# Kernel optimization log

Hardware: AMD Instinct MI355X
Metric: run time of the kernel (lower is better)

## Reference

```python
import jax, jax.numpy as jnp
import numpy as np

B, C, D, H, W = 8, 1, 160, 160, 160
SPATIAL_AXES = (2, 3, 4)  # axial, coronal, sagittal map to dims D, H, W


def setup_inputs() -> dict:
    key = jax.random.key(0)
    k1, _ = jax.random.split(key)
    x = jax.random.normal(k1, (B, C, D, H, W), dtype=jnp.float32)
    log_sigma = jnp.zeros((3,), dtype=jnp.float32)  # log(initial_sigma=1.0)
    return {"x": x, "log_sigma": log_sigma}


def reference(x, log_sigma):
    # For each spatial axis: adjacent-slice diff, squared distance summed over
    # channel + remaining spatial dims (per batch, per slice-pair), RBF kernel,
    # then -mean over (batch, slice-pairs). Equivalent to the original
    # sum_i(-mean_b(k_i)) / (n_slices - 1) since mean is linear.
    sigma = jnp.exp(log_sigma)
    total = jnp.float32(0.0)
    for i, ax in enumerate(SPATIAL_AXES):
        d = jnp.diff(x, axis=ax)  # [B, C, ...] with S-1 along ax
        reduce_dims = tuple(a for a in range(5) if a not in (0, ax))
        sq = jnp.sum(d * d, axis=reduce_dims)  # [B, S-1]
        k = jnp.exp(-sq / (2.0 * sigma[i] ** 2))
        total = total + (-jnp.mean(k))
    return total / jnp.float32(len(SPATIAL_AXES))
```

## Files before the change

kernel.cpp:

```cpp
#include <hip/hip_runtime.h>


constexpr int Wd4 = 40;
constexpr int SLICE4 = 6400;
constexpr long BSTR4 = 160L * 6400;
constexpr int NB = 8;
constexpr int NPAIR = 159;
constexpr int NKEY = 3 * NB * NPAIR;
constexpr int SLOT = 200;
constexpr int NBLK = NB * 160;
constexpr int PART_OFF = NBLK * SLOT;
constexpr int NFIN = 60;

__device__ __forceinline__ float sq4(const float4& a, const float4& c) {
    float e0 = a.x - c.x, e1 = a.y - c.y, e2 = a.z - c.z, e3 = a.w - c.w;
    return e0 * e0 + e1 * e1 + e2 * e2 + e3 * e3;
}

__global__ __launch_bounds__(320) void diff3_kernel(const float* __restrict__ x,
                                                    float* __restrict__ ws) {
    __shared__ float lds[1504];

    const int t = threadIdx.x;
    const int bid = blockIdx.x;
    const int b = bid / 160;
    const int r2 = bid % 160;
    const int ds = r2 / 5;
    const int hc = r2 % 5;
    const int d0 = ds * 5, h0 = hc * 32;
    const bool lastSeg = (ds == 31);

    const int c4 = t % 40;
    const int rp = t / 40;
    const int lane = t & 63;
    const int wv = t >> 6;
    const bool hOK = !(hc == 4 && rp == 7);
    const bool sOK = (c4 < 39);
    const bool fixB = (lane == 63) && sOK;

    const float4* base = (const float4*)x + (size_t)b * BSTR4 + (size_t)d0 * SLICE4
                       + (size_t)(h0 + 4 * rp) * Wd4 + c4;

    float aW[4] = {0.f, 0.f, 0.f, 0.f};
    float aH[4] = {0.f, 0.f, 0.f, 0.f};
    float aD[5] = {0.f, 0.f, 0.f, 0.f, 0.f};
    float4 p0, p1, p2, p3;

#pragma unroll
    for (int it = 0; it < 5; ++it) {
        const float4* sp = base + it * SLICE4;
        const float4 v0 = sp[0];
        const float4 v1 = sp[Wd4];
        const float4 v2 = sp[2 * Wd4];
        const float4 v3 = sp[3 * Wd4];
        float4 hv;
        if (hOK) hv = sp[4 * Wd4];
        float bx0 = 0.f, bx1 = 0.f, bx2 = 0.f, bx3 = 0.f;
        if (fixB) {
            bx0 = ((const float*)(sp))[4];
            bx1 = ((const float*)(sp + Wd4))[4];
            bx2 = ((const float*)(sp + 2 * Wd4))[4];
            bx3 = ((const float*)(sp + 3 * Wd4))[4];
        }
        float s0 = __shfl_down(v0.x, 1, 64); if (fixB) s0 = bx0;
        float s1 = __shfl_down(v1.x, 1, 64); if (fixB) s1 = bx1;
        float s2 = __shfl_down(v2.x, 1, 64); if (fixB) s2 = bx2;
        float s3 = __shfl_down(v3.x, 1, 64); if (fixB) s3 = bx3;

        float dw;
        dw = v0.y - v0.x; aW[0] += dw * dw;
        dw = v0.z - v0.y; aW[1] += dw * dw;
        dw = v0.w - v0.z; aW[2] += dw * dw;
        dw = v1.y - v1.x; aW[0] += dw * dw;
        dw = v1.z - v1.y; aW[1] += dw * dw;
        dw = v1.w - v1.z; aW[2] += dw * dw;
        dw = v2.y - v2.x; aW[0] += dw * dw;
        dw = v2.z - v2.y; aW[1] += dw * dw;
        dw = v2.w - v2.z; aW[2] += dw * dw;
        dw = v3.y - v3.x; aW[0] += dw * dw;
        dw = v3.z - v3.y; aW[1] += dw * dw;
        dw = v3.w - v3.z; aW[2] += dw * dw;
        if (sOK) {
            dw = s0 - v0.w; aW[3] += dw * dw;
            dw = s1 - v1.w; aW[3] += dw * dw;
            dw = s2 - v2.w; aW[3] += dw * dw;
            dw = s3 - v3.w; aW[3] += dw * dw;
        }
        aH[0] += sq4(v1, v0);
        aH[1] += sq4(v2, v1);
        aH[2] += sq4(v3, v2);
        if (hOK) aH[3] += sq4(hv, v3);
        if (it > 0)
            aD[it - 1] += sq4(v0, p0) + sq4(v1, p1) + sq4(v2, p2) + sq4(v3, p3);
        p0 = v0; p1 = v1; p2 = v2; p3 = v3;
    }
    if (!lastSeg) {
        const float4* sp = base + 5 * SLICE4;
        aD[4] = sq4(sp[0], p0) + sq4(sp[Wd4], p1) + sq4(sp[2 * Wd4], p2) + sq4(sp[3 * Wd4], p3);
    }

#pragma unroll
    for (int j = 0; j < 4; ++j) lds[(4 * rp + j) * 41 + c4] = aH[j];
#pragma unroll
    for (int j = 0; j < 5; ++j) {
        float dd = aD[j];
        for (int off = 32; off > 0; off >>= 1) dd += __shfl_down(dd, off, 64);
        if (lane == 0) lds[1472 + j * 5 + wv] = dd;
    }
    __syncthreads();
    float hsum = 0.f, dsum = 0.f;
    if (t < 32) {
        const float* src = &lds[t * 41];
        for (int i = 0; i < 40; ++i) hsum += src[i];
    }
    if (t < 5) {
        for (int w2 = 0; w2 < 5; ++w2) dsum += lds[1472 + t * 5 + w2];
    }
    __syncthreads();
#pragma unroll
    for (int j = 0; j < 4; ++j) lds[(4 * c4 + j) * 9 + rp] = aW[j];
    __syncthreads();
    float wsum = 0.f;
    if (t < 160) {
        const float* src = &lds[t * 9];
        for (int i = 0; i < 8; ++i) wsum += src[i];
    }
    float* slot = ws + (size_t)bid * SLOT;
    if (t < 5)   slot[t] = dsum;
    if (t < 32)  slot[5 + t] = hsum;
    if (t < 160) slot[37 + t] = wsum;
}

__global__ __launch_bounds__(64) void reduce_kernel(const float* __restrict__ ws,
                                                    const float* __restrict__ log_sigma,
                                                    float* __restrict__ part) {
    const int gk = blockIdx.x * 64 + threadIdx.x;
    float kv = 0.f;
    if (gk < NKEY) {
        const int a = gk / (NB * NPAIR);
        const int rem = gk % (NB * NPAIR);
        const int b = rem / NPAIR;
        const int k = rem % NPAIR;
        const float f = -0.5f * expf(-2.f * log_sigma[a]);
        const float* bb = ws + (size_t)b * 160 * SLOT;
        float val = 0.f;
        if (a == 0) {
            const int ds = k / 5, j = k % 5;
            const float* p = bb + (size_t)(ds * 5) * SLOT + j;
            for (int hc = 0; hc < 5; ++hc) val += p[hc * SLOT];
        } else if (a == 1) {
            const int hc = k / 32, kk = k % 32;
            const float* p = bb + (size_t)hc * SLOT + 5 + kk;
            for (int ds = 0; ds < 32; ++ds) val += p[(size_t)(ds * 5) * SLOT];
        } else {
            const float* p = bb + 37 + k;
            for (int i = 0; i < 160; ++i) val += p[(size_t)i * SLOT];
        }
        kv = expf(val * f);
    }
    for (int off = 32; off > 0; off >>= 1) kv += __shfl_down(kv, off, 64);
    if (threadIdx.x == 0) part[blockIdx.x] = kv;
}

__global__ __launch_bounds__(64) void final_kernel(const float* __restrict__ part,
                                                   float* __restrict__ out) {
    float v = (threadIdx.x < NFIN) ? part[threadIdx.x] : 0.f;
    for (int off = 32; off > 0; off >>= 1) v += __shfl_down(v, off, 64);
    if (threadIdx.x == 0) out[0] = -v / (float)NKEY;
}

extern "C" void kernel_launch(void* const* d_in, const int* in_sizes, int n_in,
                              void* d_out, int out_size, void* d_ws, size_t ws_size,
                              hipStream_t stream) {
    const float* x = (const float*)d_in[0];
    const float* log_sigma = (const float*)d_in[1];
    float* out = (float*)d_out;
    float* ws = (float*)d_ws;

    diff3_kernel<<<NBLK, 320, 0, stream>>>(x, ws);
    reduce_kernel<<<NFIN, 64, 0, stream>>>(ws, log_sigma, ws + PART_OFF);
    final_kernel<<<1, 64, 0, stream>>>(ws + PART_OFF, out);
}
```

Baseline: 196.5 us.

## Stage slices into LDS with async global_load_lds triple buffering and smaller tiles

Each block now works on a 16-row tile instead of a 32-row one, so there are twice as many blocks. Each D-slice is staged into a three-deep LDS ring with async global-to-LDS loads, using vmcnt waits and barriers so the next slices load while the current one is computed. The final reduction kernel is dropped: the reduce kernel atomically adds into the output, which the first kernel zeroes. This targets memory latency and one launch, at the cost of more LDS per block, more barriers, and a nondeterministic atomic sum order.

```diff
diff --git a/kernel.cpp b/kernel.cpp
--- a/kernel.cpp
+++ b/kernel.cpp
@@ -1,71 +1,93 @@
 #include <hip/hip_runtime.h>
 
 
-constexpr int Wd4 = 40;
-constexpr int SLICE4 = 6400;
-constexpr long BSTR4 = 160L * 6400;
+constexpr int WF = 160;
+constexpr int SLICEF = 160 * 160;
+constexpr long BSTRF = 160L * SLICEF;
 constexpr int NB = 8;
 constexpr int NPAIR = 159;
 constexpr int NKEY = 3 * NB * NPAIR;
-constexpr int SLOT = 200;
-constexpr int NBLK = NB * 160;
-constexpr int PART_OFF = NBLK * SLOT;
-constexpr int NFIN = 60;
+constexpr int SLOT = 184;
+constexpr int NTILE = NB * 32 * 10;
+constexpr int BUFF = 3840;
+constexpr int NRED = 60;
 
 __device__ __forceinline__ float sq4(const float4& a, const float4& c) {
     float e0 = a.x - c.x, e1 = a.y - c.y, e2 = a.z - c.z, e3 = a.w - c.w;
     return e0 * e0 + e1 * e1 + e2 * e2 + e3 * e3;
 }
 
-__global__ __launch_bounds__(320) void diff3_kernel(const float* __restrict__ x,
-                                                    float* __restrict__ ws) {
-    __shared__ float lds[1504];
+__device__ __forceinline__ void stage16(const float* g, float* l) {
+    __builtin_amdgcn_global_load_lds(
+        (const __attribute__((address_space(1))) void*)g,
+        (__attribute__((address_space(3))) void*)l, 16, 0, 0);
+}
+
+__device__ __forceinline__ void stage_slice(const float* gs, float* lb, int t, int hc) {
+    stage16(gs + t * 4, lb + t * 4);
+    stage16(gs + 1280 + t * 4, lb + 1280 + t * 4);
+    const int hoff = (hc == 9) ? 0 : 2560;
+    stage16(gs + hoff + (t % 40) * 4, lb + 2560 + t * 4);
+}
+
+__global__ __launch_bounds__(320, 4) void diff3_kernel(const float* __restrict__ x,
+                                                       float* __restrict__ ws,
+                                                       float* __restrict__ out) {
+    __shared__ float ldsf[3 * BUFF];
 
     const int t = threadIdx.x;
-    const int bid = blockIdx.x;
-    const int b = bid / 160;
-    const int r2 = bid % 160;
-    const int ds = r2 / 5;
-    const int hc = r2 % 5;
-    const int d0 = ds * 5, h0 = hc * 32;
+    const int tile = blockIdx.x;
+    const int b = tile / 320;
+    const int r2 = tile % 320;
+    const int ds = r2 / 10;
+    const int hc = r2 % 10;
+    const int d0 = ds * 5, h0 = hc * 16;
     const bool lastSeg = (ds == 31);
 
     const int c4 = t % 40;
     const int rp = t / 40;
     const int lane = t & 63;
     const int wv = t >> 6;
-    const bool hOK = !(hc == 4 && rp == 7);
     const bool sOK = (c4 < 39);
-    const bool fixB = (lane == 63) && sOK;
+    const bool hOK = !(hc == 9 && rp == 7);
 
-    const float4* base = (const float4*)x + (size_t)b * BSTR4 + (size_t)d0 * SLICE4
-                       + (size_t)(h0 + 4 * rp) * Wd4 + c4;
+    if (tile == 0 && t == 0) out[0] = 0.f;
+
+    const float* gs0 = x + (size_t)b * BSTRF + (size_t)d0 * SLICEF + (size_t)h0 * WF;
+
+    stage_slice(gs0, ldsf, t, hc);
+    stage_slice(gs0 + SLICEF, ldsf + BUFF, t, hc);
 
     float aW[4] = {0.f, 0.f, 0.f, 0.f};
-    float aH[4] = {0.f, 0.f, 0.f, 0.f};
+    float aH0 = 0.f, aH1 = 0.f;
     float aD[5] = {0.f, 0.f, 0.f, 0.f, 0.f};
-    float4 p0, p1, p2, p3;
+    float4 p0, p1;
+
+    const int r0 = 2 * rp, r1 = 2 * rp + 1;
 
 #pragma unroll
     for (int it = 0; it < 5; ++it) {
-        const float4* sp = base + it * SLICE4;
-        const float4 v0 = sp[0];
-        const float4 v1 = sp[Wd4];
-        const float4 v2 = sp[2 * Wd4];
-        const float4 v3 = sp[3 * Wd4];
+        if (it < 4 || !lastSeg) {
+            asm volatile("s_waitcnt vmcnt(3)" ::: "memory");
+        } else {
+            asm volatile("s_waitcnt vmcnt(0)" ::: "memory");
+        }
+        __builtin_amdgcn_s_barrier();
+        __builtin_amdgcn_sched_barrier(0);
+        if (it < 3 || (it == 3 && !lastSeg))
+            stage_slice(gs0 + (size_t)(it + 2) * SLICEF, ldsf + ((it + 2) % 3) * BUFF, t, hc);
+
+        const float* bp = ldsf + (it % 3) * BUFF;
+        const float4* b4 = (const float4*)bp;
+        const float4 v0 = b4[r0 * 40 + c4];
+        const float4 v1 = b4[r1 * 40 + c4];
         float4 hv;
-        if (hOK) hv = sp[4 * Wd4];
-        float bx0 = 0.f, bx1 = 0.f, bx2 = 0.f, bx3 = 0.f;
-        if (fixB) {
-            bx0 = ((const float*)(sp))[4];
-            bx1 = ((const float*)(sp + Wd4))[4];
-            bx2 = ((const float*)(sp + 2 * Wd4))[4];
-            bx3 = ((const float*)(sp + 3 * Wd4))[4];
+        if (hOK) hv = b4[(r0 + 2) * 40 + c4];
+        float s0 = 0.f, s1 = 0.f;
+        if (sOK) {
+            s0 = bp[r0 * WF + 4 * c4 + 4];
+            s1 = bp[r1 * WF + 4 * c4 + 4];
         }
-        float s0 = __shfl_down(v0.x, 1, 64); if (fixB) s0 = bx0;
-        float s1 = __shfl_down(v1.x, 1, 64); if (fixB) s1 = bx1;
-        float s2 = __shfl_down(v2.x, 1, 64); if (fixB) s2 = bx2;
-        float s3 = __shfl_down(v3.x, 1, 64); if (fixB) s3 = bx3;
 
         float dw;
         dw = v0.y - v0.x; aW[0] += dw * dw;
@@ -74,66 +96,57 @@
         dw = v1.y - v1.x; aW[0] += dw * dw;
         dw = v1.z - v1.y; aW[1] += dw * dw;
         dw = v1.w - v1.z; aW[2] += dw * dw;
-        dw = v2.y - v2.x; aW[0] += dw * dw;
-        dw = v2.z - v2.y; aW[1] += dw * dw;
-        dw = v2.w - v2.z; aW[2] += dw * dw;
-        dw = v3.y - v3.x; aW[0] += dw * dw;
-        dw = v3.z - v3.y; aW[1] += dw * dw;
-        dw = v3.w - v3.z; aW[2] += dw * dw;
         if (sOK) {
             dw = s0 - v0.w; aW[3] += dw * dw;
             dw = s1 - v1.w; aW[3] += dw * dw;
-            dw = s2 - v2.w; aW[3] += dw * dw;
-            dw = s3 - v3.w; aW[3] += dw * dw;
         }
-        aH[0] += sq4(v1, v0);
-        aH[1] += sq4(v2, v1);
-        aH[2] += sq4(v3, v2);
-        if (hOK) aH[3] += sq4(hv, v3);
-        if (it > 0)
-            aD[it - 1] += sq4(v0, p0) + sq4(v1, p1) + sq4(v2, p2) + sq4(v3, p3);
-        p0 = v0; p1 = v1; p2 = v2; p3 = v3;
+        aH0 += sq4(v1, v0);
+        if (hOK) aH1 += sq4(hv, v1);
+        if (it > 0) aD[it - 1] += sq4(v0, p0) + sq4(v1, p1);
+        p0 = v0; p1 = v1;
     }
     if (!lastSeg) {
-        const float4* sp = base + 5 * SLICE4;
-        aD[4] = sq4(sp[0], p0) + sq4(sp[Wd4], p1) + sq4(sp[2 * Wd4], p2) + sq4(sp[3 * Wd4], p3);
+        asm volatile("s_waitcnt vmcnt(0)" ::: "memory");
+        __builtin_amdgcn_s_barrier();
+        __builtin_amdgcn_sched_barrier(0);
+        const float4* b4 = (const float4*)(ldsf + 2 * BUFF);
+        aD[4] = sq4(b4[r0 * 40 + c4], p0) + sq4(b4[r1 * 40 + c4], p1);
     }
 
-#pragma unroll
-    for (int j = 0; j < 4; ++j) lds[(4 * rp + j) * 41 + c4] = aH[j];
+    __syncthreads();
+    ldsf[r0 * 41 + c4] = aH0;
+    ldsf[r1 * 41 + c4] = aH1;
 #pragma unroll
     for (int j = 0; j < 5; ++j) {
         float dd = aD[j];
         for (int off = 32; off > 0; off >>= 1) dd += __shfl_down(dd, off, 64);
-        if (lane == 0) lds[1472 + j * 5 + wv] = dd;
+        if (lane == 0) ldsf[660 + j * 5 + wv] = dd;
     }
+#pragma unroll
+    for (int j = 0; j < 4; ++j) ldsf[700 + (4 * c4 + j) * 9 + rp] = aW[j];
     __syncthreads();
-    float hsum = 0.f, dsum = 0.f;
-    if (t < 32) {
-        const float* src = &lds[t * 41];
-        for (int i = 0; i < 40; ++i) hsum += src[i];
+
+    float* slot = ws + (size_t)tile * SLOT;
+    if (t < 16) {
+        float h = 0.f;
+        for (int i = 0; i < 40; ++i) h += ldsf[t * 41 + i];
+        slot[5 + t] = h;
     }
     if (t < 5) {
-        for (int w2 = 0; w2 < 5; ++w2) dsum += lds[1472 + t * 5 + w2];
+        float d = 0.f;
+        for (int w2 = 0; w2 < 5; ++w2) d += ldsf[660 + t * 5 + w2];
+        slot[t] = d;
     }
-    __syncthreads();
-#pragma unroll
-    for (int j = 0; j < 4; ++j) lds[(4 * c4 + j) * 9 + rp] = aW[j];
-    __syncthreads();
-    float wsum = 0.f;
     if (t < 160) {
-        const float* src = &lds[t * 9];
-        for (int i = 0; i < 8; ++i) wsum += src[i];
+        float w = 0.f;
+        for (int i = 0; i < 8; ++i) w += ldsf[700 + t * 9 + i];
+        slot[21 + t] = w;
     }
-    float* slot = ws + (size_t)bid * SLOT;
-    if (t < 5)   slot[t] = dsum;
-    if (t < 32)  slot[5 + t] = hsum;
-    if (t < 160) slot[37 + t] = wsum;
 }
 
 __global__ __launch_bounds__(64) void reduce_kernel(const float* __restrict__ ws,
                                                     const float* __restrict__ log_sigma,
-                                                    float* __restrict__ part) {
+                                                    float* __restrict__ out) {
     const int gk = blockIdx.x * 64 + threadIdx.x;
     float kv = 0.f;
     if (gk < NKEY) {
@@ -142,31 +155,24 @@
         const int b = rem / NPAIR;
         const int k = rem % NPAIR;
         const float f = -0.5f * expf(-2.f * log_sigma[a]);
-        const float* bb = ws + (size_t)b * 160 * SLOT;
+        const float* wsb = ws + (size_t)b * 320 * SLOT;
         float val = 0.f;
         if (a == 0) {
-            const int ds = k / 5, j = k % 5;
-            const float* p = bb + (size_t)(ds * 5) * SLOT + j;
-            for (int hc = 0; hc < 5; ++hc) val += p[hc * SLOT];
+            const int dss = k / 5, j = k % 5;
+            const float* p = wsb + (size_t)(dss * 10) * SLOT + j;
+            for (int hcc = 0; hcc < 10; ++hcc) val += p[(size_t)hcc * SLOT];
         } else if (a == 1) {
-            const int hc = k / 32, kk = k % 32;
-            const float* p = bb + (size_t)hc * SLOT + 5 + kk;
-            for (int ds = 0; ds < 32; ++ds) val += p[(size_t)(ds * 5) * SLOT];
+            const int hcc = k / 16, kk = k % 16;
+            const float* p = wsb + (size_t)hcc * SLOT + 5 + kk;
+            for (int dss = 0; dss < 32; ++dss) val += p[(size_t)(dss * 10) * SLOT];
         } else {
-            const float* p = bb + 37 + k;
-            for (int i = 0; i < 160; ++i) val += p[(size_t)i * SLOT];
+            const float* p = wsb + 21 + k;
+            for (int i = 0; i < 320; ++i) val += p[(size_t)i * SLOT];
         }
         kv = expf(val * f);
     }
     for (int off = 32; off > 0; off >>= 1) kv += __shfl_down(kv, off, 64);
-    if (threadIdx.x == 0) part[blockIdx.x] = kv;
-}
-
-__global__ __launch_bounds__(64) void final_kernel(const float* __restrict__ part,
-                                                   float* __restrict__ out) {
-    float v = (threadIdx.x < NFIN) ? part[threadIdx.x] : 0.f;
-    for (int off = 32; off > 0; off >>= 1) v += __shfl_down(v, off, 64);
-    if (threadIdx.x == 0) out[0] = -v / (float)NKEY;
+    if (threadIdx.x == 0) atomicAdd(out, -kv / (float)NKEY);
 }
 
 extern "C" void kernel_launch(void* const* d_in, const int* in_sizes, int n_in,
@@ -177,7 +183,6 @@
     float* out = (float*)d_out;
     float* ws = (float*)d_ws;
 
-    diff3_kernel<<<NBLK, 320, 0, stream>>>(x, ws);
-    reduce_kernel<<<NFIN, 64, 0, stream>>>(ws, log_sigma, ws + PART_OFF);
-    final_kernel<<<1, 64, 0, stream>>>(ws + PART_OFF, out);
+    diff3_kernel<<<NTILE, 320, 0, stream>>>(x, ws, out);
+    reduce_kernel<<<NRED, 64, 0, stream>>>(ws, log_sigma, out);
 }
```

Result: slower. 208.2 us (+5.9%).

## Hoist all slice loads ahead of compute and fold final reduction into atomics

Applied to the files above, without the earlier changes.

The main kernel now issues every global load for its five slices, plus the next-slice halo, up front, then computes behind a sched_barrier. This gives more memory-level parallelism per thread at the cost of many more live registers. The separate final kernel is removed: the diff kernel zeroes the output and the reduce kernel atomically adds each block's scaled partial. That saves one launch but makes the float summation order nondeterministic.

```diff
diff --git a/kernel.cpp b/kernel.cpp
--- a/kernel.cpp
+++ b/kernel.cpp
@@ -9,8 +9,7 @@
 constexpr int NKEY = 3 * NB * NPAIR;
 constexpr int SLOT = 200;
 constexpr int NBLK = NB * 160;
-constexpr int PART_OFF = NBLK * SLOT;
-constexpr int NFIN = 60;
+constexpr int NRED = 60;
 
 __device__ __forceinline__ float sq4(const float4& a, const float4& c) {
     float e0 = a.x - c.x, e1 = a.y - c.y, e2 = a.z - c.z, e3 = a.w - c.w;
@@ -18,7 +17,8 @@
 }
 
 __global__ __launch_bounds__(320) void diff3_kernel(const float* __restrict__ x,
-                                                    float* __restrict__ ws) {
+                                                    float* __restrict__ ws,
+                                                    float* __restrict__ out) {
     __shared__ float lds[1504];
 
     const int t = threadIdx.x;
@@ -38,65 +38,81 @@
     const bool sOK = (c4 < 39);
     const bool fixB = (lane == 63) && sOK;
 
+    if (bid == 0 && t == 0) out[0] = 0.f;
+
     const float4* base = (const float4*)x + (size_t)b * BSTR4 + (size_t)d0 * SLICE4
                        + (size_t)(h0 + 4 * rp) * Wd4 + c4;
+
+    float4 v[5][4];
+    float4 hv[5];
+    float  bx[5][4];
+    float4 nx[4];
+#pragma unroll
+    for (int it = 0; it < 5; ++it) {
+        const float4* sp = base + it * SLICE4;
+        v[it][0] = sp[0];
+        v[it][1] = sp[Wd4];
+        v[it][2] = sp[2 * Wd4];
+        v[it][3] = sp[3 * Wd4];
+        if (hOK) hv[it] = sp[4 * Wd4];
+        if (fixB) {
+            const float* f = (const float*)sp;
+            bx[it][0] = f[4];
+            bx[it][1] = f[4 + 160];
+            bx[it][2] = f[4 + 320];
+            bx[it][3] = f[4 + 480];
+        }
+    }
+    if (!lastSeg) {
+        const float4* sp = base + 5 * SLICE4;
+        nx[0] = sp[0];
+        nx[1] = sp[Wd4];
+        nx[2] = sp[2 * Wd4];
+        nx[3] = sp[3 * Wd4];
+    }
+    __builtin_amdgcn_sched_barrier(0);
 
     float aW[4] = {0.f, 0.f, 0.f, 0.f};
     float aH[4] = {0.f, 0.f, 0.f, 0.f};
     float aD[5] = {0.f, 0.f, 0.f, 0.f, 0.f};
-    float4 p0, p1, p2, p3;
 
 #pragma unroll
     for (int it = 0; it < 5; ++it) {
-        const float4* sp = base + it * SLICE4;
-        const float4 v0 = sp[0];
-        const float4 v1 = sp[Wd4];
-        const float4 v2 = sp[2 * Wd4];
-        const float4 v3 = sp[3 * Wd4];
-        float4 hv;
-        if (hOK) hv = sp[4 * Wd4];
-        float bx0 = 0.f, bx1 = 0.f, bx2 = 0.f, bx3 = 0.f;
-        if (fixB) {
-            bx0 = ((const float*)(sp))[4];
-            bx1 = ((const float*)(sp + Wd4))[4];
-            bx2 = ((const float*)(sp + 2 * Wd4))[4];
-            bx3 = ((const float*)(sp + 3 * Wd4))[4];
-        }
-        float s0 = __shfl_down(v0.x, 1, 64); if (fixB) s0 = bx0;
-        float s1 = __shfl_down(v1.x, 1, 64); if (fixB) s1 = bx1;
-        float s2 = __shfl_down(v2.x, 1, 64); if (fixB) s2 = bx2;
-        float s3 = __shfl_down(v3.x, 1, 64); if (fixB) s3 = bx3;
+        float s0 = __shfl_down(v[it][0].x, 1, 64); if (fixB) s0 = bx[it][0];
+        float s1 = __shfl_down(v[it][1].x, 1, 64); if (fixB) s1 = bx[it][1];
+        float s2 = __shfl_down(v[it][2].x, 1, 64); if (fixB) s2 = bx[it][2];
+        float s3 = __shfl_down(v[it][3].x, 1, 64); if (fixB) s3 = bx[it][3];
 
         float dw;
-        dw = v0.y - v0.x; aW[0] += dw * dw;
-        dw = v0.z - v0.y; aW[1] += dw * dw;
-        dw = v0.w - v0.z; aW[2] += dw * dw;
-        dw = v1.y - v1.x; aW[0] += dw * dw;
-        dw = v1.z - v1.y; aW[1] += dw * dw;
-        dw = v1.w - v1.z; aW[2] += dw * dw;
-        dw = v2.y - v2.x; aW[0] += dw * dw;
-        dw = v2.z - v2.y; aW[1] += dw * dw;
-        dw = v2.w - v2.z; aW[2] += dw * dw;
-        dw = v3.y - v3.x; aW[0] += dw * dw;
-        dw = v3.z - v3.y; aW[1] += dw * dw;
-        dw = v3.w - v3.z; aW[2] += dw * dw;
+        dw = v[it][0].y - v[it][0].x; aW[0] += dw * dw;
+        dw = v[it][0].z - v[it][0].y; aW[1] += dw * dw;
+        dw = v[it][0].w - v[it][0].z; aW[2] += dw * dw;
+        dw = v[it][1].y - v[it][1].x; aW[0] += dw * dw;
+        dw = v[it][1].z - v[it][1].y; aW[1] += dw * dw;
+        dw = v[it][1].w - v[it][1].z; aW[2] += dw * dw;
+        dw = v[it][2].y - v[it][2].x; aW[0] += dw * dw;
+        dw = v[it][2].z - v[it][2].y; aW[1] += dw * dw;
+        dw = v[it][2].w - v[it][2].z; aW[2] += dw * dw;
+        dw = v[it][3].y - v[it][3].x; aW[0] += dw * dw;
+        dw = v[it][3].z - v[it][3].y; aW[1] += dw * dw;
+        dw = v[it][3].w - v[it][3].z; aW[2] += dw * dw;
         if (sOK) {
-            dw = s0 - v0.w; aW[3] += dw * dw;
-            dw = s1 - v1.w; aW[3] += dw * dw;
-            dw = s2 - v2.w; aW[3] += dw * dw;
-            dw = s3 - v3.w; aW[3] += dw * dw;
+            dw = s0 - v[it][0].w; aW[3] += dw * dw;
+            dw = s1 - v[it][1].w; aW[3] += dw * dw;
+            dw = s2 - v[it][2].w; aW[3] += dw * dw;
+            dw = s3 - v[it][3].w; aW[3] += dw * dw;
         }
-        aH[0] += sq4(v1, v0);
-        aH[1] += sq4(v2, v1);
-        aH[2] += sq4(v3, v2);
-        if (hOK) aH[3] += sq4(hv, v3);
+        aH[0] += sq4(v[it][1], v[it][0]);
+        aH[1] += sq4(v[it][2], v[it][1]);
+        aH[2] += sq4(v[it][3], v[it][2]);
+        if (hOK) aH[3] += sq4(hv[it], v[it][3]);
         if (it > 0)
-            aD[it - 1] += sq4(v0, p0) + sq4(v1, p1) + sq4(v2, p2) + sq4(v3, p3);
-        p0 = v0; p1 = v1; p2 = v2; p3 = v3;
+            aD[it - 1] += sq4(v[it][0], v[it - 1][0]) + sq4(v[it][1], v[it - 1][1])
+                        + sq4(v[it][2], v[it - 1][2]) + sq4(v[it][3], v[it - 1][3]);
     }
     if (!lastSeg) {
-        const float4* sp = base + 5 * SLICE4;
-        aD[4] = sq4(sp[0], p0) + sq4(sp[Wd4], p1) + sq4(sp[2 * Wd4], p2) + sq4(sp[3 * Wd4], p3);
+        aD[4] = sq4(nx[0], v[4][0]) + sq4(nx[1], v[4][1])
+              + sq4(nx[2], v[4][2]) + sq4(nx[3], v[4][3]);
     }
 
 #pragma unroll
@@ -133,7 +149,7 @@
 
 __global__ __launch_bounds__(64) void reduce_kernel(const float* __restrict__ ws,
                                                     const float* __restrict__ log_sigma,
-                                                    float* __restrict__ part) {
+                                                    float* __restrict__ out) {
     const int gk = blockIdx.x * 64 + threadIdx.x;
     float kv = 0.f;
     if (gk < NKEY) {
@@ -145,13 +161,13 @@
         const float* bb = ws + (size_t)b * 160 * SLOT;
         float val = 0.f;
         if (a == 0) {
-            const int ds = k / 5, j = k % 5;
-            const float* p = bb + (size_t)(ds * 5) * SLOT + j;
-            for (int hc = 0; hc < 5; ++hc) val += p[hc * SLOT];
+            const int dss = k / 5, j = k % 5;
+            const float* p = bb + (size_t)(dss * 5) * SLOT + j;
+            for (int hcc = 0; hcc < 5; ++hcc) val += p[hcc * SLOT];
         } else if (a == 1) {
-            const int hc = k / 32, kk = k % 32;
-            const float* p = bb + (size_t)hc * SLOT + 5 + kk;
-            for (int ds = 0; ds < 32; ++ds) val += p[(size_t)(ds * 5) * SLOT];
+            const int hcc = k / 32, kk = k % 32;
+            const float* p = bb + (size_t)hcc * SLOT + 5 + kk;
+            for (int dss = 0; dss < 32; ++dss) val += p[(size_t)(dss * 5) * SLOT];
         } else {
             const float* p = bb + 37 + k;
             for (int i = 0; i < 160; ++i) val += p[(size_t)i * SLOT];
@@ -159,14 +175,7 @@
         kv = expf(val * f);
     }
     for (int off = 32; off > 0; off >>= 1) kv += __shfl_down(kv, off, 64);
-    if (threadIdx.x == 0) part[blockIdx.x] = kv;
-}
-
-__global__ __launch_bounds__(64) void final_kernel(const float* __restrict__ part,
-                                                   float* __restrict__ out) {
-    float v = (threadIdx.x < NFIN) ? part[threadIdx.x] : 0.f;
-    for (int off = 32; off > 0; off >>= 1) v += __shfl_down(v, off, 64);
-    if (threadIdx.x == 0) out[0] = -v / (float)NKEY;
+    if (threadIdx.x == 0) atomicAdd(out, -kv / (float)NKEY);
 }
 
 extern "C" void kernel_launch(void* const* d_in, const int* in_sizes, int n_in,
@@ -177,7 +186,6 @@
     float* out = (float*)d_out;
     float* ws = (float*)d_ws;
 
-    diff3_kernel<<<NBLK, 320, 0, stream>>>(x, ws);
-    reduce_kernel<<<NFIN, 64, 0, stream>>>(ws, log_sigma, ws + PART_OFF);
-    final_kernel<<<1, 64, 0, stream>>>(ws + PART_OFF, out);
+    diff3_kernel<<<NBLK, 320, 0, stream>>>(x, ws, out);
+    reduce_kernel<<<NRED, 64, 0, stream>>>(ws, log_sigma, out);
 }
```

Result: slower. 200.8 us (+2.2%).

## Fuse reduction into main kernel via atomics and last-block ticket

Applied to the files above, without the earlier changes.

Replaces the per-block workspace slots plus the separate reduce and final kernels with atomicAdd accumulation into per-key sums, followed by a last-block-done ticket that computes the RBF terms and final mean. A small zero kernel clears the accumulators and ticket beforehand. The aim is to remove one launch and the strided second-pass reads of the workspace. In exchange it adds atomic contention (about 200 atomics per block), fences, and a serial tail done by a single block.

```diff
diff --git a/kernel.cpp b/kernel.cpp
--- a/kernel.cpp
+++ b/kernel.cpp
@@ -7,19 +7,25 @@
 constexpr int NB = 8;
 constexpr int NPAIR = 159;
 constexpr int NKEY = 3 * NB * NPAIR;
-constexpr int SLOT = 200;
+constexpr int PBATCH = NB * NPAIR;
 constexpr int NBLK = NB * 160;
-constexpr int PART_OFF = NBLK * SLOT;
-constexpr int NFIN = 60;
+constexpr int NZ = NKEY + 1;
 
 __device__ __forceinline__ float sq4(const float4& a, const float4& c) {
     float e0 = a.x - c.x, e1 = a.y - c.y, e2 = a.z - c.z, e3 = a.w - c.w;
     return e0 * e0 + e1 * e1 + e2 * e2 + e3 * e3;
 }
 
+__global__ __launch_bounds__(512) void zero_kernel(float* __restrict__ ws) {
+    for (int i = threadIdx.x; i < NZ; i += 512) ws[i] = 0.f;
+}
+
 __global__ __launch_bounds__(320) void diff3_kernel(const float* __restrict__ x,
-                                                    float* __restrict__ ws) {
+                                                    const float* __restrict__ log_sigma,
+                                                    float* __restrict__ ws,
+                                                    float* __restrict__ out) {
     __shared__ float lds[1504];
+    __shared__ int sTicket;
 
     const int t = threadIdx.x;
     const int bid = blockIdx.x;
@@ -125,48 +131,37 @@
         const float* src = &lds[t * 9];
         for (int i = 0; i < 8; ++i) wsum += src[i];
     }
-    float* slot = ws + (size_t)bid * SLOT;
-    if (t < 5)   slot[t] = dsum;
-    if (t < 32)  slot[5 + t] = hsum;
-    if (t < 160) slot[37 + t] = wsum;
-}
 
-__global__ __launch_bounds__(64) void reduce_kernel(const float* __restrict__ ws,
-                                                    const float* __restrict__ log_sigma,
-                                                    float* __restrict__ part) {
-    const int gk = blockIdx.x * 64 + threadIdx.x;
-    float kv = 0.f;
-    if (gk < NKEY) {
-        const int a = gk / (NB * NPAIR);
-        const int rem = gk % (NB * NPAIR);
-        const int b = rem / NPAIR;
-        const int k = rem % NPAIR;
-        const float f = -0.5f * expf(-2.f * log_sigma[a]);
-        const float* bb = ws + (size_t)b * 160 * SLOT;
-        float val = 0.f;
-        if (a == 0) {
-            const int ds = k / 5, j = k % 5;
-            const float* p = bb + (size_t)(ds * 5) * SLOT + j;
-            for (int hc = 0; hc < 5; ++hc) val += p[hc * SLOT];
-        } else if (a == 1) {
-            const int hc = k / 32, kk = k % 32;
-            const float* p = bb + (size_t)hc * SLOT + 5 + kk;
-            for (int ds = 0; ds < 32; ++ds) val += p[(size_t)(ds * 5) * SLOT];
-        } else {
-            const float* p = bb + 37 + k;
-            for (int i = 0; i < 160; ++i) val += p[(size_t)i * SLOT];
+    float* acc = ws;
+    if (t < 5 && !(lastSeg && t == 4))
+        atomicAdd(acc + (size_t)b * NPAIR + (d0 + t), dsum);
+    if (t < 32 && !(hc == 4 && t == 31))
+        atomicAdd(acc + PBATCH + (size_t)b * NPAIR + (h0 + t), hsum);
+    if (t < 159)
+        atomicAdd(acc + 2 * PBATCH + (size_t)b * NPAIR + t, wsum);
+
+    __threadfence();
+    if (t == 0) sTicket = atomicAdd((int*)(ws + NKEY), 1);
+    __syncthreads();
+    if (sTicket == NBLK - 1) {
+        __threadfence();
+        float part = 0.f;
+        for (int gk = t; gk < NKEY; gk += 320) {
+            const float val = __hip_atomic_load(acc + gk, __ATOMIC_RELAXED,
+                                                __HIP_MEMORY_SCOPE_AGENT);
+            const int a = gk / PBATCH;
+            const float f = -0.5f * expf(-2.f * log_sigma[a]);
+            part += expf(val * f);
         }
-        kv = expf(val * f);
+        for (int off = 32; off > 0; off >>= 1) part += __shfl_down(part, off, 64);
+        __syncthreads();
+        if (lane == 0) lds[wv] = part;
+        __syncthreads();
+        if (t == 0) {
+            const float tot = lds[0] + lds[1] + lds[2] + lds[3] + lds[4];
+            out[0] = -tot / (float)NKEY;
+        }
     }
-    for (int off = 32; off > 0; off >>= 1) kv += __shfl_down(kv, off, 64);
-    if (threadIdx.x == 0) part[blockIdx.x] = kv;
-}
-
-__global__ __launch_bounds__(64) void final_kernel(const float* __restrict__ part,
-                                                   float* __restrict__ out) {
-    float v = (threadIdx.x < NFIN) ? part[threadIdx.x] : 0.f;
-    for (int off = 32; off > 0; off >>= 1) v += __shfl_down(v, off, 64);
-    if (threadIdx.x == 0) out[0] = -v / (float)NKEY;
 }
 
 extern "C" void kernel_launch(void* const* d_in, const int* in_sizes, int n_in,
@@ -177,7 +172,6 @@
     float* out = (float*)d_out;
     float* ws = (float*)d_ws;
 
-    diff3_kernel<<<NBLK, 320, 0, stream>>>(x, ws);
-    reduce_kernel<<<NFIN, 64, 0, stream>>>(ws, log_sigma, ws + PART_OFF);
-    final_kernel<<<1, 64, 0, stream>>>(ws + PART_OFF, out);
+    zero_kernel<<<1, 512, 0, stream>>>(ws);
+    diff3_kernel<<<NBLK, 320, 0, stream>>>(x, log_sigma, ws, out);
 }
```

Result: slower. 305.6 us (+55.5%).
